# Performance work log

Hardware: AMD Instinct MI355X
Metric: run time of the kernel (lower is better)

The kernel has to match this reference:

```python
import jax, jax.numpy as jnp
import numpy as np


def setup_inputs() -> dict:
    key = jax.random.key(0)
    ks = jax.random.split(key, 4)
    B, T, D, U = 256, 4096, 3, 8
    d = D + 1                      # time-augmented path dimension
    sig_dim = 1 + d + d * d        # depth-2 signature incl. constant term = 21
    glorot = jax.nn.initializers.glorot_uniform()
    return {
        "inputs": jax.random.normal(ks[0], (B, T, D), jnp.float32),
        "input_kernel": glorot(ks[1], (D, 3 * U), jnp.float32),
        "recurrent_kernel": glorot(ks[2], (U, 3 * U), jnp.float32),
        "forget_kernel": glorot(ks[3], (sig_dim, U), jnp.float32),
        "bias": jnp.zeros((4 * U,), jnp.float32),
    }


def _streamed_signature_depth2(path):
    """Streamed (cumulative) truncated signature of depth 2 via Chen's identity.
    path: (B, T, d) -> (B, T, 1 + d + d*d). Entry t is the signature of path[:t+1]."""
    B, T, d = path.shape
    dx = jnp.diff(path, axis=1)                                   # (B, T-1, d)
    L1 = jnp.cumsum(dx, axis=1)                                   # level-1
    L1_prev = jnp.concatenate([jnp.zeros((B, 1, d), path.dtype), L1[:, :-1]], axis=1)
    # Chen: L2_t = L2_{t-1} + L1_{t-1} (x) dx_t + 0.5 dx_t (x) dx_t
    terms = L1_prev[..., :, None] * dx[..., None, :] + 0.5 * dx[..., :, None] * dx[..., None, :]
    L2 = jnp.cumsum(terms, axis=1).reshape(B, T - 1, d * d)       # level-2
    sig = jnp.concatenate([jnp.ones((B, T - 1, 1), path.dtype), L1, L2], axis=-1)
    sig0 = jnp.concatenate(
        [jnp.ones((B, 1, 1), path.dtype), jnp.zeros((B, 1, d + d * d), path.dtype)], axis=-1)
    return jnp.concatenate([sig0, sig], axis=1)                   # (B, T, sig_dim)


def reference(inputs, input_kernel, recurrent_kernel, forget_kernel, bias):
    B, T, D = inputs.shape
    U = recurrent_kernel.shape[0]
    t_grid = jnp.linspace(0.0, 1.0, T)
    path = jnp.concatenate(
        [jnp.broadcast_to(t_grid[None, :, None], (B, T, 1)), inputs], axis=-1)
    sig = _streamed_signature_depth2(path)                        # (B, T, sig_dim)
    # normalize signatures at times t>0 by elapsed time (as in the original)
    sig = sig.at[:, 1:, :].set(sig[:, 1:, :] / t_grid[1:, None])

    b_i, b_f, b_c, b_o = jnp.split(bias, 4)
    x_proj = jnp.einsum('btd,du->btu', inputs, input_kernel)      # (B, T, 3U)

    def step(carry, xs):
        h, c = carry
        x_t, sig_t = xs
        gates = h @ recurrent_kernel + x_t                        # (B, 3U)
        i_t, c_hat, o_t = jnp.split(gates, 3, axis=-1)
        f_t = jax.nn.sigmoid(sig_t @ forget_kernel + b_f)         # signature forget gate
        i_t = jax.nn.sigmoid(i_t + b_i)
        c_hat = jnp.tanh(c_hat + b_c)
        o_t = jax.nn.sigmoid(o_t + b_o)
        c_new = f_t * c + i_t * c_hat
        h_new = o_t * jnp.tanh(c_new)
        return (h_new, c_new), h_new

    h0 = jnp.zeros((B, U), inputs.dtype)
    (_, _), h_seq = jax.lax.scan(
        step, (h0, h0), (x_proj.transpose(1, 0, 2), sig.transpose(1, 0, 2)))
    return h_seq.transpose(1, 0, 2)                               # (B, T, U)
```

## Files before the change

kernel.cpp:

```cpp
#include <hip/hip_runtime.h>
#include <hip/hip_bf16.h>

#define TT 4096
#define BB 256
#define DD 3
#define UU 8

#if defined(__has_builtin)
#if __has_builtin(__builtin_amdgcn_exp2f) && __has_builtin(__builtin_amdgcn_rcpf)
#define FAST_EXP2(x) __builtin_amdgcn_exp2f(x)
#define FAST_RCP(x)  __builtin_amdgcn_rcpf(x)
#endif
#endif
#ifndef FAST_EXP2
#define FAST_EXP2(x) exp2f(x)
#define FAST_RCP(x)  (1.0f / (x))
#endif

#define NLOG2E  (-1.4426950408889634f)
#define P2LOG2E ( 2.8853900817779268f)

__device__ __forceinline__ float fsig(float x) {
    float e = FAST_EXP2(NLOG2E * x);
    return FAST_RCP(1.0f + e);
}

template <int CTRL>
__device__ __forceinline__ float dpp_f(float v) {
    int i = __builtin_bit_cast(int, v);
    i = __builtin_amdgcn_update_dpp(0, i, CTRL, 0xF, 0xF, true);
    return __builtin_bit_cast(float, i);
}
template <int CTRL, int RM>
__device__ __forceinline__ float dpp_add(float x) {
    int t = __builtin_amdgcn_update_dpp(0, __builtin_bit_cast(int, x), CTRL, RM, 0xF, true);
    return x + __builtin_bit_cast(float, t);
}
__device__ __forceinline__ float wave_incl_scan(float v) {
    v = dpp_add<0x111, 0xF>(v);
    v = dpp_add<0x112, 0xF>(v);
    v = dpp_add<0x114, 0xF>(v);
    v = dpp_add<0x118, 0xF>(v);
    v = dpp_add<0x142, 0xA>(v);
    v = dpp_add<0x143, 0xC>(v);
    return v;
}

__global__ __launch_bounds__(256) void sig_pre_kernel(
    const float* __restrict__ x,
    const float* __restrict__ Wi,
    const float* __restrict__ Wf,
    const float* __restrict__ bias,
    float* __restrict__ ws)
{
    __shared__ float sWf[168];
    __shared__ float sWi[72];
    __shared__ float sB[32];
    __shared__ float tot1[4 * 4];
    __shared__ float tot2[4 * 16];

    const int tid = threadIdx.x;
    const int b = blockIdx.x;
    if (tid < 168) sWf[tid] = NLOG2E * Wf[tid];
    if (tid < 72) {
        int col = tid % 24;
        float s = (col < 8) ? NLOG2E : (col < 16) ? P2LOG2E : NLOG2E;
        sWi[tid] = s * Wi[tid];
    }
    if (tid < 32) {
        float s = (tid < 16) ? NLOG2E : (tid < 24) ? P2LOG2E : NLOG2E;
        sB[tid] = s * bias[tid];
    }
    __syncthreads();

    const float dtc = 1.0f / 4095.0f;
    const int t0 = tid * 16;
    const int lid = tid & 63;
    const int wv = tid >> 6;
    const float* xb = x + (size_t)b * TT * DD;

    float xs[48];
    {
        const float4* xv = (const float4*)(xb + (size_t)t0 * 3);
        #pragma unroll
        for (int k = 0; k < 12; ++k) {
            float4 v = xv[k];
            xs[k * 4 + 0] = v.x; xs[k * 4 + 1] = v.y;
            xs[k * 4 + 2] = v.z; xs[k * 4 + 3] = v.w;
        }
    }
    float pp0, pp1, pp2;
    if (tid == 0) { pp0 = xs[0]; pp1 = xs[1]; pp2 = xs[2]; }
    else { pp0 = xb[t0 * 3 - 3]; pp1 = xb[t0 * 3 - 2]; pp2 = xb[t0 * 3 - 1]; }

    float l1[4] = {0.f, 0.f, 0.f, 0.f};
    float l2[16];
    #pragma unroll
    for (int i = 0; i < 16; ++i) l2[i] = 0.f;
    {
        float xp0 = pp0, xp1 = pp1, xp2 = pp2;
        #pragma unroll
        for (int i = 0; i < 16; ++i) {
            float c0 = xs[i * 3], c1 = xs[i * 3 + 1], c2 = xs[i * 3 + 2];
            float d0 = (tid == 0 && i == 0) ? 0.f : dtc;
            float dxv[4] = {d0, c0 - xp0, c1 - xp1, c2 - xp2};
            #pragma unroll
            for (int r = 0; r < 4; ++r) {
                float tr = l1[r] + 0.5f * dxv[r];
                #pragma unroll
                for (int cc = 0; cc < 4; ++cc)
                    l2[r * 4 + cc] = fmaf(tr, dxv[cc], l2[r * 4 + cc]);
            }
            #pragma unroll
            for (int r = 0; r < 4; ++r) l1[r] += dxv[r];
            xp0 = c0; xp1 = c1; xp2 = c2;
        }
    }

    float I1[4], O1[4];
    #pragma unroll
    for (int r = 0; r < 4; ++r) {
        I1[r] = wave_incl_scan(l1[r]);
        if (lid == 63) tot1[wv * 4 + r] = I1[r];
    }
    __syncthreads();
    #pragma unroll
    for (int r = 0; r < 4; ++r) {
        float off = 0.f;
        for (int w = 0; w < wv; ++w) off += tot1[w * 4 + r];
        O1[r] = off + I1[r] - l1[r];
    }

    float I2[16], cin[16], O2[16];
    #pragma unroll
    for (int rc = 0; rc < 16; ++rc) {
        float c2v = l2[rc] + O1[rc >> 2] * l1[rc & 3];
        cin[rc] = c2v;
        I2[rc] = wave_incl_scan(c2v);
        if (lid == 63) tot2[wv * 16 + rc] = I2[rc];
    }
    __syncthreads();
    #pragma unroll
    for (int rc = 0; rc < 16; ++rc) {
        float off = 0.f;
        for (int w = 0; w < wv; ++w) off += tot2[w * 16 + rc];
        O2[rc] = off + I2[rc] - cin[rc];
    }

    #pragma unroll
    for (int r = 0; r < 4; ++r) l1[r] = O1[r];
    #pragma unroll
    for (int i = 0; i < 16; ++i) l2[i] = O2[i];

    float xp0 = pp0, xp1 = pp1, xp2 = pp2;
    #pragma unroll
    for (int i2 = 0; i2 < 16; ++i2) {
        const int t = t0 + i2;
        float c0 = xs[i2 * 3], c1 = xs[i2 * 3 + 1], c2 = xs[i2 * 3 + 2];
        float d0 = (tid == 0 && i2 == 0) ? 0.f : dtc;
        float dxv[4] = {d0, c0 - xp0, c1 - xp1, c2 - xp2};
        #pragma unroll
        for (int r = 0; r < 4; ++r) {
            float tr = l1[r] + 0.5f * dxv[r];
            #pragma unroll
            for (int cc = 0; cc < 4; ++cc)
                l2[r * 4 + cc] = fmaf(tr, dxv[cc], l2[r * 4 + cc]);
        }
        #pragma unroll
        for (int r = 0; r < 4; ++r) l1[r] += dxv[r];
        xp0 = c0; xp1 = c1; xp2 = c2;

        const float scale = (t == 0) ? 1.0f : (4095.0f / (float)t);
        float fa[8];
        #pragma unroll
        for (int u = 0; u < 8; ++u) fa[u] = sWf[u];
        #pragma unroll
        for (int r = 0; r < 4; ++r) {
            float s = l1[r];
            #pragma unroll
            for (int u = 0; u < 8; ++u) fa[u] = fmaf(s, sWf[(1 + r) * 8 + u], fa[u]);
        }
        #pragma unroll
        for (int rc = 0; rc < 16; ++rc) {
            float s = l2[rc];
            #pragma unroll
            for (int u = 0; u < 8; ++u) fa[u] = fmaf(s, sWf[(5 + rc) * 8 + u], fa[u]);
        }
        float g[24];
        #pragma unroll
        for (int u = 0; u < 8; ++u) {
            g[u] = sB[u]; g[8 + u] = sB[16 + u]; g[16 + u] = sB[24 + u];
        }
        #pragma unroll
        for (int gg = 0; gg < 24; ++gg) {
            g[gg] = fmaf(c0, sWi[gg], g[gg]);
            g[gg] = fmaf(c1, sWi[24 + gg], g[gg]);
            g[gg] = fmaf(c2, sWi[48 + gg], g[gg]);
        }
        float4* wp = (float4*)ws + ((size_t)t * BB + b) * UU;
        #pragma unroll
        for (int u = 0; u < 8; ++u) {
            float fav = fmaf(scale, fa[u], sB[8 + u]);
            float f = FAST_RCP(1.0f + FAST_EXP2(fav));
            wp[u] = make_float4(g[u], g[8 + u], g[16 + u], f);
        }
    }
}

__global__ __launch_bounds__(64) void lstm_scan_full(
    const float* __restrict__ ws, const float* __restrict__ Wr,
    float* __restrict__ out)
{
    const int lane = threadIdx.x;
    const int u = lane & 7;
    const int b = blockIdx.x * 8 + (lane >> 3);
    float wa[8], wb[8], wc[8];
    #pragma unroll
    for (int m = 0; m < 8; ++m) {
        int j = u ^ m;
        wa[m] = NLOG2E  * Wr[j * 24 + u];
        wb[m] = P2LOG2E * Wr[j * 24 + 8 + u];
        wc[m] = NLOG2E  * Wr[j * 24 + 16 + u];
    }
    const float4* gp = (const float4*)ws + (size_t)b * 8 + u;
    float4 buf[8];
    #pragma unroll
    for (int p = 0; p < 8; ++p) buf[p] = gp[(size_t)p * 2048];
    float h = 0.f, c = 0.f;
    float* op = out + (size_t)b * TT * 8 + u;

    auto step = [&](int t, float4 g) {
        float h1 = dpp_f<0xB1>(h);
        float h2 = dpp_f<0x4E>(h);
        float h3 = dpp_f<0x1B>(h);
        float h7 = dpp_f<0x141>(h);
        float h6 = dpp_f<0xB1>(h7);
        float h5 = dpp_f<0x4E>(h7);
        float h4 = dpp_f<0x1B>(h7);
        float gi = fmaf(h, wa[0], g.x), giB = h4 * wa[4];
        float gc = fmaf(h, wb[0], g.y), gcB = h4 * wb[4];
        float go = fmaf(h, wc[0], g.z), goB = h4 * wc[4];
        gi = fmaf(h1, wa[1], gi);  giB = fmaf(h5, wa[5], giB);
        gc = fmaf(h1, wb[1], gc);  gcB = fmaf(h5, wb[5], gcB);
        go = fmaf(h1, wc[1], go);  goB = fmaf(h5, wc[5], goB);
        gi = fmaf(h2, wa[2], gi);  giB = fmaf(h6, wa[6], giB);
        gc = fmaf(h2, wb[2], gc);  gcB = fmaf(h6, wb[6], gcB);
        go = fmaf(h2, wc[2], go);  goB = fmaf(h6, wc[6], goB);
        gi = fmaf(h3, wa[3], gi);  giB = fmaf(h7, wa[7], giB);
        gc = fmaf(h3, wb[3], gc);  gcB = fmaf(h7, wb[7], gcB);
        go = fmaf(h3, wc[3], go);  goB = fmaf(h7, wc[7], goB);
        gi += giB; gc += gcB; go += goB;
        float ei = FAST_EXP2(gi);
        float ec = FAST_EXP2(gc);
        float eo = FAST_EXP2(go);
        float r1 = FAST_RCP((1.0f + ei) * (1.0f + ec));
        c = fmaf(g.w, c, (ec - 1.0f) * r1);
        float s3 = fminf(P2LOG2E * c, 63.0f);
        float e2c = FAST_EXP2(s3);
        float r2 = FAST_RCP((1.0f + eo) * (1.0f + e2c));
        h = (e2c - 1.0f) * r2;
        op[(size_t)t * 8] = h;
    };

    for (int tb = 0; tb + 8 < TT; tb += 8) {
        #pragma unroll
        for (int j = 0; j < 8; ++j) {
            const int t = tb + j;
            float4 g = buf[j];
            buf[j] = gp[(size_t)(t + 8) * 2048];
            step(t, g);
        }
    }
    #pragma unroll
    for (int j = 0; j < 8; ++j) step(TT - 8 + j, buf[j]);
}

__global__ __launch_bounds__(64) void lstm_scan_ultra(
    const float* __restrict__ x, const float* __restrict__ Wi,
    const float* __restrict__ Wr, const float* __restrict__ Wf,
    const float* __restrict__ bias, float* __restrict__ out)
{
    const int lane = threadIdx.x;
    const int u = lane & 7;
    const int q = lane >> 3;
    const int b = blockIdx.x * 8 + q;
    float wa[8], wb[8], wc[8];
    #pragma unroll
    for (int m = 0; m < 8; ++m) {
        int j = u ^ m;
        wa[m] = Wr[j * 24 + u];
        wb[m] = Wr[j * 24 + 8 + u];
        wc[m] = Wr[j * 24 + 16 + u];
    }
    float wia[3], wib[3], wic[3];
    #pragma unroll
    for (int k = 0; k < 3; ++k) {
        wia[k] = Wi[k * 24 + u];
        wib[k] = Wi[k * 24 + 8 + u];
        wic[k] = Wi[k * 24 + 16 + u];
    }
    float wf[21];
    #pragma unroll
    for (int j = 0; j < 21; ++j) wf[j] = Wf[j * 8 + u];
    const float bi = bias[u], bf = bias[8 + u], bc = bias[16 + u], bo = bias[24 + u];
    const float* xb = x + (size_t)b * TT * 3;
    float l1[4] = {0.f, 0.f, 0.f, 0.f};
    float l2[16];
    #pragma unroll
    for (int i = 0; i < 16; ++i) l2[i] = 0.f;
    float xp0 = xb[0], xp1 = xb[1], xp2 = xb[2];
    float h = 0.f, c = 0.f;
    float* op = out + (size_t)b * TT * 8 + u;
    const float dtc = 1.0f / 4095.0f;
    for (int t = 0; t < TT; ++t) {
        float c0 = xb[t * 3 + 0], c1 = xb[t * 3 + 1], c2 = xb[t * 3 + 2];
        if (t > 0) {
            float dxv[4] = {dtc, c0 - xp0, c1 - xp1, c2 - xp2};
            #pragma unroll
            for (int r = 0; r < 4; ++r) {
                float tr = l1[r] + 0.5f * dxv[r];
                #pragma unroll
                for (int cc = 0; cc < 4; ++cc)
                    l2[r * 4 + cc] = fmaf(tr, dxv[cc], l2[r * 4 + cc]);
            }
            #pragma unroll
            for (int r = 0; r < 4; ++r) l1[r] += dxv[r];
        }
        xp0 = c0; xp1 = c1; xp2 = c2;
        const float scale = (t == 0) ? 1.0f : (4095.0f / (float)t);
        float dot = wf[0];
        #pragma unroll
        for (int r = 0; r < 4; ++r) dot = fmaf(l1[r], wf[1 + r], dot);
        #pragma unroll
        for (int rc = 0; rc < 16; ++rc) dot = fmaf(l2[rc], wf[5 + rc], dot);
        float fv = fsig(fmaf(scale, dot, bf));
        float gi = bi, gc = bc, go = bo;
        gi = fmaf(c0, wia[0], gi); gi = fmaf(c1, wia[1], gi); gi = fmaf(c2, wia[2], gi);
        gc = fmaf(c0, wib[0], gc); gc = fmaf(c1, wib[1], gc); gc = fmaf(c2, wib[2], gc);
        go = fmaf(c0, wic[0], go); go = fmaf(c1, wic[1], go); go = fmaf(c2, wic[2], go);
        float h1 = dpp_f<0xB1>(h);
        float h2 = dpp_f<0x4E>(h);
        float h3 = dpp_f<0x1B>(h);
        float h7 = dpp_f<0x141>(h);
        float h6 = dpp_f<0xB1>(h7);
        float h5 = dpp_f<0x4E>(h7);
        float h4 = dpp_f<0x1B>(h7);
        gi = fmaf(h, wa[0], gi); gi = fmaf(h1, wa[1], gi); gi = fmaf(h2, wa[2], gi); gi = fmaf(h3, wa[3], gi);
        gi = fmaf(h4, wa[4], gi); gi = fmaf(h5, wa[5], gi); gi = fmaf(h6, wa[6], gi); gi = fmaf(h7, wa[7], gi);
        gc = fmaf(h, wb[0], gc); gc = fmaf(h1, wb[1], gc); gc = fmaf(h2, wb[2], gc); gc = fmaf(h3, wb[3], gc);
        gc = fmaf(h4, wb[4], gc); gc = fmaf(h5, wb[5], gc); gc = fmaf(h6, wb[6], gc); gc = fmaf(h7, wb[7], gc);
        go = fmaf(h, wc[0], go); go = fmaf(h1, wc[1], go); go = fmaf(h2, wc[2], go); go = fmaf(h3, wc[3], go);
        go = fmaf(h4, wc[4], go); go = fmaf(h5, wc[5], go); go = fmaf(h6, wc[6], go); go = fmaf(h7, wc[7], go);
        float iv = fsig(gi);
        float cv = 1.0f - 2.0f * FAST_RCP(1.0f + FAST_EXP2(P2LOG2E * gc));
        float ov = fsig(go);
        c = fmaf(fv, c, iv * cv);
        float s3 = fminf(P2LOG2E * c, 63.0f);
        h = ov * (1.0f - 2.0f * FAST_RCP(1.0f + FAST_EXP2(s3)));
        op[(size_t)t * 8] = h;
    }
}

extern "C" void kernel_launch(void* const* d_in, const int* in_sizes, int n_in,
                              void* d_out, int out_size, void* d_ws, size_t ws_size,
                              hipStream_t stream) {
    const float* x    = (const float*)d_in[0];
    const float* Wi   = (const float*)d_in[1];
    const float* Wr   = (const float*)d_in[2];
    const float* Wf   = (const float*)d_in[3];
    const float* bias = (const float*)d_in[4];
    float* out = (float*)d_out;

    const size_t need = (size_t)TT * BB * UU * 4 * sizeof(float);
    if (ws_size >= need) {
        sig_pre_kernel<<<dim3(BB), dim3(256), 0, stream>>>(x, Wi, Wf, bias, (float*)d_ws);
        lstm_scan_full<<<dim3(BB / 8), dim3(64), 0, stream>>>((const float*)d_ws, Wr, out);
    } else {
        lstm_scan_ultra<<<dim3(BB / 8), dim3(64), 0, stream>>>(x, Wi, Wr, Wf, bias, out);
    }
}
```

Baseline: 784.7 us.

## Split signature precompute across 1024 threads and restructure LSTM gate activations

The signature precompute kernel now gives each thread 4 timesteps instead of 16 and launches 1024 threads per batch row. This shortens the serial per-thread work and register footprint, at the cost of more cross-wave prefix-sum steps. The scan register arrays are trimmed. In the serial LSTM recurrence, the fused shared-reciprocal gate math is replaced by three separate reciprocals and the clamp on the tanh exponent is removed. That shortens the dependency chain but adds reciprocal instructions and risks inf/NaN handling at large |c|.

```diff
diff --git a/kernel.cpp b/kernel.cpp
--- a/kernel.cpp
+++ b/kernel.cpp
@@ -46,7 +46,8 @@
     return v;
 }
 
-__global__ __launch_bounds__(256) void sig_pre_kernel(
+#define CH 4
+__global__ __launch_bounds__(1024) void sig_pre_kernel(
     const float* __restrict__ x,
     const float* __restrict__ Wi,
     const float* __restrict__ Wf,
@@ -56,8 +57,8 @@
     __shared__ float sWf[168];
     __shared__ float sWi[72];
     __shared__ float sB[32];
-    __shared__ float tot1[4 * 4];
-    __shared__ float tot2[4 * 16];
+    __shared__ float tot1[16 * 4];
+    __shared__ float tot2[16 * 16];
 
     const int tid = threadIdx.x;
     const int b = blockIdx.x;
@@ -74,16 +75,16 @@
     __syncthreads();
 
     const float dtc = 1.0f / 4095.0f;
-    const int t0 = tid * 16;
+    const int t0 = tid * CH;
     const int lid = tid & 63;
     const int wv = tid >> 6;
     const float* xb = x + (size_t)b * TT * DD;
 
-    float xs[48];
+    float xs[CH * 3];
     {
         const float4* xv = (const float4*)(xb + (size_t)t0 * 3);
         #pragma unroll
-        for (int k = 0; k < 12; ++k) {
+        for (int k = 0; k < 3; ++k) {
             float4 v = xv[k];
             xs[k * 4 + 0] = v.x; xs[k * 4 + 1] = v.y;
             xs[k * 4 + 2] = v.z; xs[k * 4 + 3] = v.w;
@@ -100,7 +101,7 @@
     {
         float xp0 = pp0, xp1 = pp1, xp2 = pp2;
         #pragma unroll
-        for (int i = 0; i < 16; ++i) {
+        for (int i = 0; i < CH; ++i) {
             float c0 = xs[i * 3], c1 = xs[i * 3 + 1], c2 = xs[i * 3 + 2];
             float d0 = (tid == 0 && i == 0) ? 0.f : dtc;
             float dxv[4] = {d0, c0 - xp0, c1 - xp1, c2 - xp2};
@@ -131,20 +132,20 @@
         O1[r] = off + I1[r] - l1[r];
     }
 
-    float I2[16], cin[16], O2[16];
+    float O2[16];
     #pragma unroll
     for (int rc = 0; rc < 16; ++rc) {
         float c2v = l2[rc] + O1[rc >> 2] * l1[rc & 3];
-        cin[rc] = c2v;
-        I2[rc] = wave_incl_scan(c2v);
-        if (lid == 63) tot2[wv * 16 + rc] = I2[rc];
+        float I2 = wave_incl_scan(c2v);
+        if (lid == 63) tot2[wv * 16 + rc] = I2;
+        O2[rc] = I2 - c2v;
     }
     __syncthreads();
     #pragma unroll
     for (int rc = 0; rc < 16; ++rc) {
         float off = 0.f;
         for (int w = 0; w < wv; ++w) off += tot2[w * 16 + rc];
-        O2[rc] = off + I2[rc] - cin[rc];
+        O2[rc] += off;
     }
 
     #pragma unroll
@@ -154,7 +155,7 @@
 
     float xp0 = pp0, xp1 = pp1, xp2 = pp2;
     #pragma unroll
-    for (int i2 = 0; i2 < 16; ++i2) {
+    for (int i2 = 0; i2 < CH; ++i2) {
         const int t = t0 + i2;
         float c0 = xs[i2 * 3], c1 = xs[i2 * 3 + 1], c2 = xs[i2 * 3 + 2];
         float d0 = (tid == 0 && i2 == 0) ? 0.f : dtc;
@@ -253,12 +254,13 @@
         float ei = FAST_EXP2(gi);
         float ec = FAST_EXP2(gc);
         float eo = FAST_EXP2(go);
-        float r1 = FAST_RCP((1.0f + ei) * (1.0f + ec));
-        c = fmaf(g.w, c, (ec - 1.0f) * r1);
-        float s3 = fminf(P2LOG2E * c, 63.0f);
-        float e2c = FAST_EXP2(s3);
-        float r2 = FAST_RCP((1.0f + eo) * (1.0f + e2c));
-        h = (e2c - 1.0f) * r2;
+        float iv = FAST_RCP(1.0f + ei);
+        float cv = fmaf(-2.0f, FAST_RCP(1.0f + ec), 1.0f);
+        float ov = FAST_RCP(1.0f + eo);
+        c = fmaf(g.w, c, iv * cv);
+        float e2 = FAST_EXP2(P2LOG2E * c);
+        float ct = fmaf(-2.0f, FAST_RCP(1.0f + e2), 1.0f);
+        h = ov * ct;
         op[(size_t)t * 8] = h;
     };
 
@@ -355,8 +357,7 @@
         float cv = 1.0f - 2.0f * FAST_RCP(1.0f + FAST_EXP2(P2LOG2E * gc));
         float ov = fsig(go);
         c = fmaf(fv, c, iv * cv);
-        float s3 = fminf(P2LOG2E * c, 63.0f);
-        h = ov * (1.0f - 2.0f * FAST_RCP(1.0f + FAST_EXP2(s3)));
+        h = ov * (1.0f - 2.0f * FAST_RCP(1.0f + FAST_EXP2(P2LOG2E * c)));
         op[(size_t)t * 8] = h;
     }
 }
@@ -373,7 +374,7 @@
 
     const size_t need = (size_t)TT * BB * UU * 4 * sizeof(float);
     if (ws_size >= need) {
-        sig_pre_kernel<<<dim3(BB), dim3(256), 0, stream>>>(x, Wi, Wf, bias, (float*)d_ws);
+        sig_pre_kernel<<<dim3(BB), dim3(1024), 0, stream>>>(x, Wi, Wf, bias, (float*)d_ws);
         lstm_scan_full<<<dim3(BB / 8), dim3(64), 0, stream>>>((const float*)d_ws, Wr, out);
     } else {
         lstm_scan_ultra<<<dim3(BB / 8), dim3(64), 0, stream>>>(x, Wi, Wr, Wf, bias, out);
```

New measurement: 1.200 ms. +52.9%, slower.
